# Optimization experiments

Measured on AMD Instinct MI355X. Metric: run time of the kernel, lower is better.

## Reference

```python
import jax, jax.numpy as jnp
import numpy as np

EPS = 1e-8


def setup_inputs() -> dict:
    key = jax.random.key(0)
    ks = jax.random.split(key, 9)
    b, f, n1, n2 = 32, 256, 64, 256
    inp = {
        "search_feats": jax.random.normal(ks[0], (b, f, n2), jnp.float32),
        "template_feats": jax.random.normal(ks[1], (b, f, n1), jnp.float32),
        "template_seeds": jax.random.normal(ks[2], (b, n1, 3), jnp.float32),
        # SharedMLP (1x1 conv2d) weights: channels 260 -> 256 -> 256 -> 256
        "W1": jax.random.normal(ks[3], (256, 260), jnp.float32) * 0.05,
        "b1": jnp.zeros((256,), jnp.float32),
        "W2": jax.random.normal(ks[4], (256, 256), jnp.float32) * 0.05,
        "b2": jnp.zeros((256,), jnp.float32),
        "W3": jax.random.normal(ks[5], (256, 256), jnp.float32) * 0.05,
        "b3": jnp.zeros((256,), jnp.float32),
        # conv1d chain (kernel size 1): 256 -> 256 (ReLU) -> 256 (no act)
        "W4": jax.random.normal(ks[6], (256, 256), jnp.float32) * 0.05,
        "b4": jnp.zeros((256,), jnp.float32),
        "W5": jax.random.normal(ks[7], (256, 256), jnp.float32) * 0.05,
        "b5": jnp.zeros((256,), jnp.float32),
    }
    return inp


def reference(search_feats, template_feats, template_seeds,
              W1, b1, W2, b2, W3, b3, W4, b4, W5, b5):
    b, f, n2 = search_feats.shape
    n1 = template_feats.shape[-1]

    # Cosine similarity along feature dim (torch clamps each norm to eps).
    t_norm = template_feats / jnp.maximum(
        jnp.linalg.norm(template_feats, axis=1, keepdims=True), EPS)
    s_norm = search_feats / jnp.maximum(
        jnp.linalg.norm(search_feats, axis=1, keepdims=True), EPS)
    sim = jnp.einsum('bfn,bfm->bnm', t_norm, s_norm)  # (b, n1, n2)

    # Build fusion feature (b, 1+3+f, n1, n2) via broadcasting (no copies needed).
    xyz = jnp.transpose(template_seeds, (0, 2, 1))  # (b, 3, n1)
    xyz_b = jnp.broadcast_to(xyz[:, :, :, None], (b, 3, n1, n2))
    tf_b = jnp.broadcast_to(template_feats[:, :, :, None], (b, f, n1, n2))
    fusion = jnp.concatenate([sim[:, None], xyz_b, tf_b], axis=1)  # (b, 260, n1, n2)

    # SharedMLP: 1x1 conv2d + ReLU per layer
    x = jax.nn.relu(jnp.einsum('oc,bcnm->bonm', W1, fusion) + b1[None, :, None, None])
    x = jax.nn.relu(jnp.einsum('oc,bcnm->bonm', W2, x) + b2[None, :, None, None])
    x = jax.nn.relu(jnp.einsum('oc,bcnm->bonm', W3, x) + b3[None, :, None, None])

    # max_pool2d over n1 dim (kernel [n1, 1]) then squeeze -> (b, 256, n2)
    x = jnp.max(x, axis=2)

    # conv1d chain (kernel size 1)
    x = jax.nn.relu(jnp.einsum('oc,bcm->bom', W4, x) + b4[None, :, None])
    x = jnp.einsum('oc,bcm->bom', W5, x) + b5[None, :, None]
    return x
```

## Files before the change

kernel.cpp:

```cpp
#include <hip/hip_runtime.h>
#include <math.h>

#define BB 32
#define FF 256
#define N1 64
#define N2 256

typedef _Float16 f16;
typedef _Float16 f16x4 __attribute__((ext_vector_type(4)));
typedef _Float16 f16x8 __attribute__((ext_vector_type(8)));
typedef float f32x4 __attribute__((ext_vector_type(4)));

#define OFFB_W14T 0u
#define OFFB_W1H  45056u
#define OFFB_W2H  176128u
#define OFFB_W3H  307200u
#define OFFB_W4H  438272u
#define OFFB_W5H  569344u

__global__ void k_prep(const float* __restrict__ W1, const float* __restrict__ W2,
                       const float* __restrict__ W3, const float* __restrict__ W4,
                       const float* __restrict__ W5, char* __restrict__ wsb) {
  int x = blockIdx.x, m = blockIdx.y, t = threadIdx.x;
  int idx = x * 256 + t;
  if (m == 0)      ((f16*)(wsb + OFFB_W2H))[idx] = (f16)W2[idx];
  else if (m == 1) ((f16*)(wsb + OFFB_W3H))[idx] = (f16)W3[idx];
  else if (m == 2) ((f16*)(wsb + OFFB_W4H))[idx] = (f16)W4[idx];
  else if (m == 3) ((f16*)(wsb + OFFB_W5H))[idx] = (f16)W5[idx];
  else if (m == 4) ((f16*)(wsb + OFFB_W1H))[idx] = (f16)W1[x * 260 + 4 + t];
  else if (x < 4)  ((float*)(wsb + OFFB_W14T))[x * 256 + t] = W1[t * 260 + x];
}


#define ZERO_ACC                                                  \
  _Pragma("unroll") for (int of = 0; of < 2; ++of)                \
  _Pragma("unroll") for (int mf = 0; mf < 2; ++mf)                \
      acc[of][mf] = (f32x4){0.f, 0.f, 0.f, 0.f};

#define GEMM2(SRC)                                                                \
  {                                                                               \
    f16x8 bfa0 = *(const f16x8*)((SRC) + 0 * 1024 + lane * 16);                   \
    f16x8 bfa1 = *(const f16x8*)((SRC) + 1 * 1024 + lane * 16);                   \
    __builtin_amdgcn_s_setprio(1);                                                \
    _Pragma("unroll") for (int ks = 0; ks < 8; ++ks) {                            \
      f16x8 bfb0 = bfa0, bfb1 = bfa1;                                             \
      if (ks < 7) {                                                               \
        bfb0 = *(const f16x8*)((SRC) + ((ks + 1) * 2 + 0) * 1024 + lane * 16);    \
        bfb1 = *(const f16x8*)((SRC) + ((ks + 1) * 2 + 1) * 1024 + lane * 16);    \
      }                                                                           \
      _Pragma("unroll") for (int of = 0; of < 2; ++of) {                          \
        acc[of][0] = __builtin_amdgcn_mfma_f32_16x16x32_f16(wreg[of][ks], bfa0,   \
                                                            acc[of][0], 0, 0, 0); \
        acc[of][1] = __builtin_amdgcn_mfma_f32_16x16x32_f16(wreg[of][ks], bfa1,   \
                                                            acc[of][1], 0, 0, 0); \
      }                                                                           \
      bfa0 = bfb0; bfa1 = bfb1;                                                   \
    }                                                                             \
    __builtin_amdgcn_s_setprio(0);                                                \
  }

#define LOAD_WREG(WH)                                                             \
  _Pragma("unroll") for (int of = 0; of < 2; ++of)                                \
  _Pragma("unroll") for (int ks = 0; ks < 8; ++ks)                                \
      wreg[of][ks] = *(const f16x8*)((WH) + (wg * 32 + of * 16 + r) * 256 +       \
                                     ks * 32 + g * 8);

#define STORE_FRAG(DST, BIASP)                                                    \
  _Pragma("unroll") for (int of = 0; of < 2; ++of) {                              \
    f32x4 bv = *(const f32x4*)((BIASP) + wg * 32 + of * 16 + g * 4);              \
    _Pragma("unroll") for (int mf = 0; mf < 2; ++mf) {                            \
      f16x4 hv;                                                                   \
      _Pragma("unroll") for (int j = 0; j < 4; ++j)                               \
          hv[j] = (f16)fmaxf(acc[of][mf][j] + bv[j], 0.f);                        \
      *(f16x4*)((DST) + (wg * 2 + mf) * 1024 + (of * 2 + (g >> 1)) * 256 +        \
                r * 16 + (g & 1) * 8) = hv;                                       \
    }                                                                             \
  }

#define POOLUP(BIASP)                                                             \
  _Pragma("unroll") for (int of = 0; of < 2; ++of) {                              \
    f32x4 bv = *(const f32x4*)((BIASP) + wg * 32 + of * 16 + g * 4);              \
    _Pragma("unroll") for (int mf = 0; mf < 2; ++mf)                              \
    _Pragma("unroll") for (int j = 0; j < 4; ++j) {                               \
      f16 hv = (f16)fmaxf(acc[of][mf][j] + bv[j], 0.f);                           \
      if (hv > pool[of][mf][j]) pool[of][mf][j] = hv;                             \
    }                                                                             \
  }

#define PRODUCE_Y1(NN, DST)                                                       \
  {                                                                               \
    float simv = sml[(NN) * 32 + mp * 16 + r];                                    \
    f16x8 c8 = *(const f16x8*)(c1h + (NN) * 264 + kp * 32 + g * 8);               \
    f16x8 h;                                                                      \
    _Pragma("unroll") for (int q = 0; q < 4; ++q) {                               \
      h[q] = (f16)fmaxf(fmaf(w1a[q], simv, (float)c8[q]), 0.f);                   \
      h[4 + q] = (f16)fmaxf(fmaf(w1b[q], simv, (float)c8[4 + q]), 0.f);           \
    }                                                                             \
    *(f16x8*)((DST) + w * 1024 + lane * 16) = h;                                  \
  }

__global__ __launch_bounds__(1024, 4) void k_mega(
    const float* __restrict__ sf, const float* __restrict__ tf,
    const float* __restrict__ seeds, const float* __restrict__ b1,
    const float* __restrict__ b2, const float* __restrict__ b3,
    const float* __restrict__ b4, const float* __restrict__ b5,
    const char* __restrict__ wsb, float* __restrict__ out) {
  const int mt = blockIdx.x, b = blockIdx.y, mb = mt * 32;
  const int tid = threadIdx.x;
  const int w = tid >> 6, lane = tid & 63, g = lane >> 4, r = lane & 15;
  const int grp = w >> 3, wg = w & 7;
  const int kp = w >> 1, mp = w & 1;

  const float* w14t = (const float*)(wsb + OFFB_W14T);
  const f16* w1h = (const f16*)(wsb + OFFB_W1H);
  const f16* w2h = (const f16*)(wsb + OFFB_W2H);
  const f16* w3h = (const f16*)(wsb + OFFB_W3H);
  const f16* w4h = (const f16*)(wsb + OFFB_W4H);
  const f16* w5h = (const f16*)(wsb + OFFB_W5H);

  __shared__ __align__(16) char arena[112384];
#define Y1BUF(i) (arena + (i) * 16384)
#define Y2BUF(i) (arena + 32768 + (i) * 16384)
  f16* c1h = (f16*)(arena + 65536);
  float* sml = (float*)(arena + 99328);
  float* blds = (float*)(arena + 107520);
  float* invt_l = (float*)(arena + 111616);
  float* invs_l = (float*)(arena + 111872);
  float* part_t = (float*)(arena + 49152);
  float* part_s = (float*)(arena + 53248);

  {
    const int n = tid & 63, fo = tid >> 6;
    float ssq = 0.f;
#pragma unroll
    for (int j = 0; j < 2; ++j) {
      int oct = j * 16 + fo;
      f16x8 h;
#pragma unroll
      for (int e = 0; e < 8; ++e) {
        float v = tf[((size_t)b * FF + oct * 8 + e) * N1 + n];
        ssq = fmaf(v, v, ssq);
        h[e] = (f16)v;
      }
      *(f16x8*)(arena + ((oct >> 2) * 4 + (n >> 4)) * 1024 +
                ((oct & 3) * 16 + (n & 15)) * 16) = h;
    }
    part_t[n * 16 + fo] = ssq;
  }
  {
    const int m = tid & 31, q = tid >> 5;
    float ssq = 0.f;
    f16x8 h;
#pragma unroll
    for (int e = 0; e < 8; ++e) {
      float v = sf[((size_t)b * FF + q * 8 + e) * N2 + mb + m];
      ssq = fmaf(v, v, ssq);
      h[e] = (f16)v;
    }
    *(f16x8*)(arena + 32768 + ((q >> 2) * 2 + (m >> 4)) * 1024 +
              ((q & 3) * 16 + (m & 15)) * 16) = h;
    part_s[m * 32 + q] = ssq;
  }
  if (tid < 256) {
    blds[tid] = b2[tid];
    blds[256 + tid] = b3[tid];
    blds[512 + tid] = b4[tid];
    blds[768 + tid] = b5[tid];
  }
  __syncthreads();
  if (tid < 64) {
    float a = 0.f;
#pragma unroll
    for (int i = 0; i < 16; ++i) a += part_t[tid * 16 + i];
    invt_l[tid] = 1.0f / fmaxf(sqrtf(a), 1e-8f);
  }
  if (tid < 32) {
    float a = 0.f;
#pragma unroll
    for (int i = 0; i < 32; ++i) a += part_s[tid * 32 + i];
    invs_l[tid] = 1.0f / fmaxf(sqrtf(a), 1e-8f);
  }
  __syncthreads();

  if (w < 8) {
    const int nt = w >> 1, mfs = w & 1;
    f32x4 sa = {0.f, 0.f, 0.f, 0.f};
#pragma unroll
    for (int ks = 0; ks < 8; ++ks) {
      f16x8 af = *(const f16x8*)(arena + (ks * 4 + nt) * 1024 + lane * 16);
      f16x8 bfm = *(const f16x8*)(arena + 32768 + (ks * 2 + mfs) * 1024 + lane * 16);
      sa = __builtin_amdgcn_mfma_f32_16x16x32_f16(af, bfm, sa, 0, 0, 0);
    }
    float ivm = invs_l[mfs * 16 + r];
#pragma unroll
    for (int j = 0; j < 4; ++j) {
      int n = nt * 16 + g * 4 + j;
      sml[n * 32 + mfs * 16 + r] = sa[j] * invt_l[n] * ivm;
    }
  }
  {
    f32x4 ac[4];
#pragma unroll
    for (int nf = 0; nf < 4; ++nf) ac[nf] = (f32x4){0.f, 0.f, 0.f, 0.f};
#pragma unroll 1
    for (int half = 0; half < 2; ++half) {
      f16x8 w1f[4];
#pragma unroll
      for (int kk = 0; kk < 4; ++kk)
        w1f[kk] = *(const f16x8*)(w1h + (w * 16 + r) * 256 +
                                  (half * 4 + kk) * 32 + g * 8);
#pragma unroll
      for (int kk = 0; kk < 4; ++kk)
#pragma unroll
        for (int nf = 0; nf < 4; ++nf) {
          f16x8 bfm = *(const f16x8*)(arena + ((half * 4 + kk) * 4 + nf) * 1024 +
                                      lane * 16);
          ac[nf] =
              __builtin_amdgcn_mfma_f32_16x16x32_f16(w1f[kk], bfm, ac[nf], 0, 0, 0);
        }
    }
    f32x4 b1v = *(const f32x4*)(b1 + w * 16 + g * 4);
    f32x4 wx = *(const f32x4*)(w14t + 256 + w * 16 + g * 4);
    f32x4 wy = *(const f32x4*)(w14t + 512 + w * 16 + g * 4);
    f32x4 wz = *(const f32x4*)(w14t + 768 + w * 16 + g * 4);
#pragma unroll
    for (int nf = 0; nf < 4; ++nf) {
      int n = nf * 16 + r;
      const float* sd = seeds + ((size_t)b * 64 + n) * 3;
      float sx = sd[0], sy = sd[1], sz = sd[2];
      f16x4 hv;
#pragma unroll
      for (int j = 0; j < 4; ++j)
        hv[j] = (f16)(ac[nf][j] + b1v[j] + wx[j] * sx + wy[j] * sy + wz[j] * sz);
      *(f16x4*)(c1h + n * 264 + w * 16 + g * 4) = hv;
    }
  }
  __syncthreads();

  f16x8 wreg[2][8];
  f16x4 pool[2][2];
  f32x4 acc[2][2];
  f32x4 w1a, w1b;
  if (grp) { LOAD_WREG(w3h); } else { LOAD_WREG(w2h); }
  w1a = *(const f32x4*)(w14t + kp * 32 + g * 8);
  w1b = *(const f32x4*)(w14t + kp * 32 + g * 8 + 4);
#pragma unroll
  for (int of = 0; of < 2; ++of)
#pragma unroll
    for (int mf = 0; mf < 2; ++mf) pool[of][mf] = (f16x4){0, 0, 0, 0};

  PRODUCE_Y1(0, Y1BUF(0));
  __syncthreads();

  const float* bA = blds;
  const float* bB = blds + 256;

  for (int n = 0; n < N1; ++n) {
    if (grp == 0) {
      ZERO_ACC;
      GEMM2(Y1BUF(n & 1));
      STORE_FRAG(Y2BUF(n & 1), bA);
      if (n + 1 < N1) PRODUCE_Y1(n + 1, Y1BUF((n + 1) & 1));
    } else {
      if (n + 1 < N1) PRODUCE_Y1(n + 1, Y1BUF((n + 1) & 1));
      if (n > 0) {
        ZERO_ACC;
        GEMM2(Y2BUF((n - 1) & 1));
        POOLUP(bB);
      }
    }
    __syncthreads();
  }

  if (grp == 1) {
    ZERO_ACC;
    GEMM2(Y2BUF(1));
    POOLUP(bB);
#pragma unroll
    for (int of = 0; of < 2; ++of)
#pragma unroll
      for (int mf = 0; mf < 2; ++mf)
        *(f16x4*)(Y1BUF(0) + (wg * 2 + mf) * 1024 + (of * 2 + (g >> 1)) * 256 +
                  r * 16 + (g & 1) * 8) = pool[of][mf];
  } else {
    LOAD_WREG(w4h);
  }
  __syncthreads();
  if (grp == 0) {
    ZERO_ACC;
    GEMM2(Y1BUF(0));
    STORE_FRAG(Y2BUF(0), blds + 512);
  } else {
    LOAD_WREG(w5h);
  }
  __syncthreads();
  if (grp == 1) {
    ZERO_ACC;
    GEMM2(Y2BUF(0));
#pragma unroll
    for (int of = 0; of < 2; ++of) {
      f32x4 bv = *(const f32x4*)(blds + 768 + wg * 32 + of * 16 + g * 4);
#pragma unroll
      for (int mf = 0; mf < 2; ++mf) {
        float* op = out + ((size_t)(b * 256 + wg * 32 + of * 16 + g * 4)) * 256 +
                    mb + mf * 16 + r;
#pragma unroll
        for (int j = 0; j < 4; ++j)
          op[(size_t)j * 256] = acc[of][mf][j] + bv[j];
      }
    }
  }
}

extern "C" void kernel_launch(void* const* d_in, const int* in_sizes, int n_in,
                              void* d_out, int out_size, void* d_ws, size_t ws_size,
                              hipStream_t stream) {
  const float* sf = (const float*)d_in[0];
  const float* tf = (const float*)d_in[1];
  const float* seeds = (const float*)d_in[2];
  const float* W1 = (const float*)d_in[3];
  const float* b1 = (const float*)d_in[4];
  const float* W2 = (const float*)d_in[5];
  const float* b2 = (const float*)d_in[6];
  const float* W3 = (const float*)d_in[7];
  const float* b3 = (const float*)d_in[8];
  const float* W4 = (const float*)d_in[9];
  const float* b4 = (const float*)d_in[10];
  const float* W5 = (const float*)d_in[11];
  const float* b5 = (const float*)d_in[12];
  char* wsb = (char*)d_ws;
  float* out = (float*)d_out;

  k_prep<<<dim3(256, 6), 256, 0, stream>>>(W1, W2, W3, W4, W5, wsb);
  k_mega<<<dim3(8, BB), 1024, 0, stream>>>(sf, tf, seeds, b1, b2, b3, b4, b5,
                                           wsb, out);
}
```

Before: 135.3 us.

## Process two template rows per barrier with quad-buffered LDS and global C1 staging

The main n1 loop now handles two rows per iteration, with four-deep Y1/Y2 LDS ring buffers, so the number of block-wide barriers is halved. The per-batch layer-1 partial (c1) moves from LDS into a global workspace region. The next two rows of c1 are prefetched into registers at the top of each iteration, which frees LDS for the deeper buffering. In exchange it uses more LDS and extra global traffic. It also relies on the workspace being large enough for the new C1 region.

```diff
diff --git a/kernel.cpp b/kernel.cpp
--- a/kernel.cpp
+++ b/kernel.cpp
@@ -17,6 +17,7 @@
 #define OFFB_W3H  307200u
 #define OFFB_W4H  438272u
 #define OFFB_W5H  569344u
+#define OFFB_C1G  700416u
 
 __global__ void k_prep(const float* __restrict__ W1, const float* __restrict__ W2,
                        const float* __restrict__ W3, const float* __restrict__ W4,
@@ -87,16 +88,15 @@
     }                                                                             \
   }
 
-#define PRODUCE_Y1(NN, DST)                                                       \
+#define PRODUCE_ROW(NN, C8)                                                       \
   {                                                                               \
     float simv = sml[(NN) * 32 + mp * 16 + r];                                    \
-    f16x8 c8 = *(const f16x8*)(c1h + (NN) * 264 + kp * 32 + g * 8);               \
     f16x8 h;                                                                      \
     _Pragma("unroll") for (int q = 0; q < 4; ++q) {                               \
-      h[q] = (f16)fmaxf(fmaf(w1a[q], simv, (float)c8[q]), 0.f);                   \
-      h[4 + q] = (f16)fmaxf(fmaf(w1b[q], simv, (float)c8[4 + q]), 0.f);           \
+      h[q] = (f16)fmaxf(fmaf(w1a[q], simv, (float)(C8)[q]), 0.f);                 \
+      h[4 + q] = (f16)fmaxf(fmaf(w1b[q], simv, (float)(C8)[4 + q]), 0.f);         \
     }                                                                             \
-    *(f16x8*)((DST) + w * 1024 + lane * 16) = h;                                  \
+    *(f16x8*)(Y1S(NN) + w * 1024 + lane * 16) = h;                                \
   }
 
 __global__ __launch_bounds__(1024, 4) void k_mega(
@@ -104,7 +104,7 @@
     const float* __restrict__ seeds, const float* __restrict__ b1,
     const float* __restrict__ b2, const float* __restrict__ b3,
     const float* __restrict__ b4, const float* __restrict__ b5,
-    const char* __restrict__ wsb, float* __restrict__ out) {
+    char* __restrict__ wsb, float* __restrict__ out) {
   const int mt = blockIdx.x, b = blockIdx.y, mb = mt * 32;
   const int tid = threadIdx.x;
   const int w = tid >> 6, lane = tid & 63, g = lane >> 4, r = lane & 15;
@@ -117,17 +117,17 @@
   const f16* w3h = (const f16*)(wsb + OFFB_W3H);
   const f16* w4h = (const f16*)(wsb + OFFB_W4H);
   const f16* w5h = (const f16*)(wsb + OFFB_W5H);
-
-  __shared__ __align__(16) char arena[112384];
-#define Y1BUF(i) (arena + (i) * 16384)
-#define Y2BUF(i) (arena + 32768 + (i) * 16384)
-  f16* c1h = (f16*)(arena + 65536);
-  float* sml = (float*)(arena + 99328);
-  float* blds = (float*)(arena + 107520);
-  float* invt_l = (float*)(arena + 111616);
-  float* invs_l = (float*)(arena + 111872);
-  float* part_t = (float*)(arena + 49152);
-  float* part_s = (float*)(arena + 53248);
+  f16* c1b = (f16*)(wsb + OFFB_C1G) + (size_t)b * 16384;
+
+  __shared__ __align__(16) char arena[143744];
+#define Y1S(n) (arena + ((n) & 3) * 16384)
+#define Y2S(n) (arena + 65536 + ((n) & 3) * 16384)
+  float* sml = (float*)(arena + 131072);
+  float* blds = (float*)(arena + 139264);
+  float* invt_l = (float*)(arena + 143360);
+  float* invs_l = (float*)(arena + 143616);
+  float* part_t = (float*)(arena + 98304);
+  float* part_s = (float*)(arena + 102400);
 
   {
     const int n = tid & 63, fo = tid >> 6;
@@ -157,7 +157,7 @@
       ssq = fmaf(v, v, ssq);
       h[e] = (f16)v;
     }
-    *(f16x8*)(arena + 32768 + ((q >> 2) * 2 + (m >> 4)) * 1024 +
+    *(f16x8*)(arena + 65536 + ((q >> 2) * 2 + (m >> 4)) * 1024 +
               ((q & 3) * 16 + (m & 15)) * 16) = h;
     part_s[m * 32 + q] = ssq;
   }
@@ -188,7 +188,7 @@
 #pragma unroll
     for (int ks = 0; ks < 8; ++ks) {
       f16x8 af = *(const f16x8*)(arena + (ks * 4 + nt) * 1024 + lane * 16);
-      f16x8 bfm = *(const f16x8*)(arena + 32768 + (ks * 2 + mfs) * 1024 + lane * 16);
+      f16x8 bfm = *(const f16x8*)(arena + 65536 + (ks * 2 + mfs) * 1024 + lane * 16);
       sa = __builtin_amdgcn_mfma_f32_16x16x32_f16(af, bfm, sa, 0, 0, 0);
     }
     float ivm = invs_l[mfs * 16 + r];
@@ -232,7 +232,7 @@
 #pragma unroll
       for (int j = 0; j < 4; ++j)
         hv[j] = (f16)(ac[nf][j] + b1v[j] + wx[j] * sx + wy[j] * sy + wz[j] * sz);
-      *(f16x4*)(c1h + n * 264 + w * 16 + g * 4) = hv;
+      *(f16x4*)(c1b + n * 256 + w * 16 + g * 4) = hv;
     }
   }
   __syncthreads();
@@ -249,38 +249,58 @@
 #pragma unroll
     for (int mf = 0; mf < 2; ++mf) pool[of][mf] = (f16x4){0, 0, 0, 0};
 
-  PRODUCE_Y1(0, Y1BUF(0));
+  {
+    f16x8 c80 = *(const f16x8*)(c1b + 0 * 256 + kp * 32 + g * 8);
+    f16x8 c81 = *(const f16x8*)(c1b + 1 * 256 + kp * 32 + g * 8);
+    PRODUCE_ROW(0, c80);
+    PRODUCE_ROW(1, c81);
+  }
   __syncthreads();
 
   const float* bA = blds;
   const float* bB = blds + 256;
 
-  for (int n = 0; n < N1; ++n) {
+  for (int p = 0; p < 32; ++p) {
+    const int n0 = 2 * p;
+    f16x8 c8a, c8b;
+    if (p < 31) {
+      c8a = *(const f16x8*)(c1b + (n0 + 2) * 256 + kp * 32 + g * 8);
+      c8b = *(const f16x8*)(c1b + (n0 + 3) * 256 + kp * 32 + g * 8);
+    }
     if (grp == 0) {
       ZERO_ACC;
-      GEMM2(Y1BUF(n & 1));
-      STORE_FRAG(Y2BUF(n & 1), bA);
-      if (n + 1 < N1) PRODUCE_Y1(n + 1, Y1BUF((n + 1) & 1));
+      GEMM2(Y1S(n0));
+      STORE_FRAG(Y2S(n0), bA);
+      ZERO_ACC;
+      GEMM2(Y1S(n0 + 1));
+      STORE_FRAG(Y2S(n0 + 1), bA);
+      if (p < 31) { PRODUCE_ROW(n0 + 2, c8a); PRODUCE_ROW(n0 + 3, c8b); }
     } else {
-      if (n + 1 < N1) PRODUCE_Y1(n + 1, Y1BUF((n + 1) & 1));
-      if (n > 0) {
+      if (p > 0) {
         ZERO_ACC;
-        GEMM2(Y2BUF((n - 1) & 1));
+        GEMM2(Y2S(n0 - 2));
+        POOLUP(bB);
+        ZERO_ACC;
+        GEMM2(Y2S(n0 - 1));
         POOLUP(bB);
       }
+      if (p < 31) { PRODUCE_ROW(n0 + 2, c8a); PRODUCE_ROW(n0 + 3, c8b); }
     }
     __syncthreads();
   }
 
   if (grp == 1) {
     ZERO_ACC;
-    GEMM2(Y2BUF(1));
+    GEMM2(Y2S(62));
     POOLUP(bB);
+    ZERO_ACC;
+    GEMM2(Y2S(63));
+    POOLUP(bB);
 #pragma unroll
     for (int of = 0; of < 2; ++of)
 #pragma unroll
       for (int mf = 0; mf < 2; ++mf)
-        *(f16x4*)(Y1BUF(0) + (wg * 2 + mf) * 1024 + (of * 2 + (g >> 1)) * 256 +
+        *(f16x4*)(Y1S(0) + (wg * 2 + mf) * 1024 + (of * 2 + (g >> 1)) * 256 +
                   r * 16 + (g & 1) * 8) = pool[of][mf];
   } else {
     LOAD_WREG(w4h);
@@ -288,15 +308,15 @@
   __syncthreads();
   if (grp == 0) {
     ZERO_ACC;
-    GEMM2(Y1BUF(0));
-    STORE_FRAG(Y2BUF(0), blds + 512);
+    GEMM2(Y1S(0));
+    STORE_FRAG(Y2S(0), blds + 512);
   } else {
     LOAD_WREG(w5h);
   }
   __syncthreads();
   if (grp == 1) {
     ZERO_ACC;
-    GEMM2(Y2BUF(0));
+    GEMM2(Y2S(0));
 #pragma unroll
     for (int of = 0; of < 2; ++of) {
       f32x4 bv = *(const f32x4*)(blds + 768 + wg * 32 + of * 16 + g * 4);
```

New measurement: 142.5 us. +5.3%, slower.
